# Kernel tuning notes

Measured on AMD Instinct MI355X. Metric: run time of the kernel, lower is better.

## Reference

```python
import jax, jax.numpy as jnp
import numpy as np

N_NODES, N_EDGES, H = 25000, 400000, 64
EPS = 1e-15


def _norm(x):
    return jnp.sqrt(jnp.sum(x * x, axis=-1, keepdims=True))


def _projx(x, c):
    norm = _norm(x)
    max_norm = (1.0 - 1e-5) / jnp.sqrt(c)
    scale = jnp.minimum(max_norm / jnp.maximum(norm, EPS), 1.0)
    return x * scale


def _expmap0(x, c):
    norm = _norm(x)
    sc = jnp.sqrt(c)
    return jnp.tanh(sc * norm) * x / (norm * sc + EPS)


def _logmap0(x, c):
    norm = _norm(x)
    sc = jnp.sqrt(c)
    return (1.0 / sc) * jnp.arctanh(jnp.minimum(sc * norm, 1.0 - 1e-5)) * x / (norm + EPS)


def _mobius_add(x, y, c):
    x2 = jnp.sum(x * x, axis=-1, keepdims=True)
    y2 = jnp.sum(y * y, axis=-1, keepdims=True)
    xy = jnp.sum(x * y, axis=-1, keepdims=True)
    num = (1.0 + 2.0 * c * xy + c * y2) * x + (1.0 - c * x2) * y
    denom = 1.0 + 2.0 * c * xy + c * c * x2 * y2
    return num / (denom + EPS)


def _mobius_linear(x, W, b, c):
    t = _logmap0(x, c)
    out = t @ W.T + b
    return _expmap0(out, c)


def setup_inputs() -> dict:
    key = jax.random.key(0)
    ks = jax.random.split(key, 12)
    h_V = jax.random.normal(ks[0], (N_NODES, H), dtype=jnp.float32) * 0.3
    h_E = jax.random.normal(ks[1], (N_EDGES, 3 * H), dtype=jnp.float32) * 0.3
    src = jax.random.randint(ks[2], (N_EDGES,), 0, N_NODES, dtype=jnp.int32)
    dst = jax.random.randint(ks[3], (N_EDGES,), 0, N_NODES, dtype=jnp.int32)
    log_c = jnp.zeros((), dtype=jnp.float32)  # c = 1.0

    def lin(k, out_d, in_d):
        bound = 1.0 / np.sqrt(in_d)
        kw, kb = jax.random.split(k)
        W = jax.random.uniform(kw, (out_d, in_d), jnp.float32, -bound, bound)
        b = jax.random.uniform(kb, (out_d,), jnp.float32, -bound, bound)
        return W, b

    W1_w, W1_b = lin(ks[4], H, 5 * H)
    W2_w, W2_b = lin(ks[5], H, H)
    W3_w, W3_b = lin(ks[6], H, H)
    return {"h_V": h_V, "h_E": h_E, "src": src, "dst": dst, "log_c": log_c,
            "W1_w": W1_w, "W1_b": W1_b, "W2_w": W2_w, "W2_b": W2_b,
            "W3_w": W3_w, "W3_b": W3_b}


def reference(h_V, h_E, src, dst, log_c, W1_w, W1_b, W2_w, W2_b, W3_w, W3_b):
    c = jnp.exp(log_c)
    n_nodes = h_V.shape[0]
    h_E = _projx(h_E, c)
    h_V = _projx(h_V, c)
    # edge gather -> fused mobius-linear chain  [E, 5H] -> [E, H]
    h_EV = jnp.concatenate([h_E, h_V[src], h_V[dst]], axis=-1)
    h_EV = _mobius_linear(h_EV, W1_w, W1_b, c)
    h_EV = _mobius_linear(_projx(jax.nn.relu(h_EV), c), W2_w, W2_b, c)
    h_msg = _mobius_linear(_projx(jax.nn.relu(h_EV), c), W3_w, W3_b, c)
    # hyperbolic aggregate: logmap0 -> scatter-mean over src -> expmap0
    tangent = _logmap0(h_msg, c)
    sums = jax.ops.segment_sum(tangent, src, num_segments=n_nodes)
    counts = jax.ops.segment_sum(jnp.ones((tangent.shape[0],), tangent.dtype), src,
                                 num_segments=n_nodes)
    agg_t = sums / jnp.maximum(counts, 1.0)[:, None]
    agg = _expmap0(agg_t, c)
    h_V = _mobius_add(h_V, agg, c)  # dropout disabled (eval)
    return _projx(h_V, c)
```

## Files before the change

### kernel.cpp

```cpp
#include <hip/hip_runtime.h>
#include <hip/hip_bf16.h>
#include <math.h>

#define EPSF 1e-15f

typedef __attribute__((ext_vector_type(8))) short bf16x8;
typedef __attribute__((ext_vector_type(4))) float f32x4;

__device__ __forceinline__ unsigned short f2bf(float x) {
    unsigned u = __float_as_uint(x);
    u += 0x7fffu + ((u >> 16) & 1u);
    return (unsigned short)(u >> 16);
}
__device__ __forceinline__ float bf2f(unsigned short b) {
    return __uint_as_float(((unsigned)b) << 16);
}
__device__ __forceinline__ unsigned pkbf(float lo, float hi) {
    __hip_bfloat162 h = __float22bfloat162_rn(make_float2(lo, hi));
    return *reinterpret_cast<unsigned*>(&h);
}
__device__ __forceinline__ float fast_tanh_pos(float x) {
    if (x < 0.25f) { float x2 = x * x; return x * (1.0f - x2 * (0.33333334f - 0.13333334f * x2)); }
    float e = __expf(2.0f * x);
    return 1.0f - 2.0f / (e + 1.0f);
}
__device__ __forceinline__ float fast_atanh01(float y) {
    if (y < 0.125f) { float y2 = y * y; return y * (1.0f + y2 * (0.33333334f + 0.2f * y2)); }
    return 0.5f * __logf((1.0f + y) / (1.0f - y));
}

__device__ __forceinline__ float wred(float v) {
#pragma unroll
    for (int off = 32; off; off >>= 1) v += __shfl_xor(v, off);
    return v;
}

__global__ void prep_wfrag(const float* __restrict__ W1, const float* __restrict__ W2,
                           const float* __restrict__ W3, unsigned short* __restrict__ Wf) {
    int idx = blockIdx.x * blockDim.x + threadIdx.x;
    if (idx >= 56 * 64) return;
    int fid = idx >> 6, lane = idx & 63;
    int i15 = lane & 15, grp = lane >> 4;
    const float* srcW; int ks, t, ld;
    if (fid < 40)      { srcW = W1; ks = fid >> 2;        t = fid & 3; ld = 320; }
    else if (fid < 48) { srcW = W2; ks = (fid - 40) >> 2; t = fid & 3; ld = 64; }
    else               { srcW = W3; ks = (fid - 48) >> 2; t = fid & 3; ld = 64; }
    int col = t * 16 + i15;
    int k0  = ks * 32 + grp * 8;
    unsigned short* dstp = Wf + ((size_t)fid * 64 + lane) * 8;
#pragma unroll
    for (int i = 0; i < 8; ++i) dstp[i] = f2bf(srcW[col * ld + k0 + i]);
}

__global__ void __launch_bounds__(256)
node_prep(const float* __restrict__ hV, const float* __restrict__ logc,
          unsigned short* __restrict__ hVp, float* __restrict__ pj, int n_nodes) {
    int wid  = (blockIdx.x * blockDim.x + threadIdx.x) >> 6;
    int lane = threadIdx.x & 63;
    if (wid >= n_nodes) return;
    float c    = __expf(logc[0]);
    float scq  = sqrtf(c);
    float maxn = (1.0f - 1e-5f) / scq;
    float x = hV[(size_t)wid * 64 + lane];
    float p = wred(x * x);
    float sS = fminf(maxn / fmaxf(sqrtf(p), EPSF), 1.0f);
    hVp[(size_t)wid * 64 + lane] = f2bf(x * sS);
    if (lane == 0) pj[wid] = sS * sS * p;
}

__global__ void hist_kernel(const int* __restrict__ src, int* __restrict__ cnt,
                            int* __restrict__ slot, int n_edges) {
    int e = blockIdx.x * blockDim.x + threadIdx.x;
    if (e < n_edges) slot[e] = atomicAdd(&cnt[src[e]], 1);
}

__global__ void __launch_bounds__(1024)
scan_rowptr(const int* __restrict__ cnt, int* __restrict__ rowptr, int n) {
    __shared__ int wpart[16];
    int C   = (n + 1023) >> 10;
    int tid = threadIdx.x;
    int beg = tid * C;
    int end = beg + C; if (end > n) end = n;
    int s = 0;
    if (beg < n) for (int k = beg; k < end; ++k) s += cnt[k];
    int lane = tid & 63, wv = tid >> 6;
    int v = s;
#pragma unroll
    for (int off = 1; off < 64; off <<= 1) {
        int t = __shfl_up(v, off);
        if (lane >= off) v += t;
    }
    if (lane == 63) wpart[wv] = v;
    __syncthreads();
    if (tid < 64) {
        int t = (tid < 16) ? wpart[tid] : 0;
#pragma unroll
        for (int off = 1; off < 16; off <<= 1) {
            int u = __shfl_up(t, off);
            if (lane >= off) t += u;
        }
        if (tid < 16) wpart[tid] = t;
    }
    __syncthreads();
    int base = (wv ? wpart[wv - 1] : 0) + (v - s);
    if (beg < n) {
        int run = base;
        for (int k = beg; k < end; ++k) { rowptr[k] = run; run += cnt[k]; }
    }
    if (tid == 1023) rowptr[n] = wpart[15];
}

__global__ void slotfix_kernel(const int* __restrict__ src, const int* __restrict__ rowptr,
                               int* __restrict__ slot, int n_edges) {
    int e = blockIdx.x * blockDim.x + threadIdx.x;
    if (e < n_edges) slot[e] += rowptr[src[e]];
}

__device__ __forceinline__ void stage_mlp(float (&v)[4][4], unsigned short* tb,
                                          const bf16x8* __restrict__ Wfrag, int fbase,
                                          const float* __restrict__ bvec,
                                          float scq, float maxn, int lane) {
    int i15 = lane & 15, grp = lane >> 4;
    float n2[4], rn2[4];
#pragma unroll
    for (int r = 0; r < 4; ++r) {
        float s = 0.f;
#pragma unroll
        for (int t = 0; t < 4; ++t) s = fmaf(v[t][r], v[t][r], s);
        n2[r] = s;
    }
#pragma unroll
    for (int r = 0; r < 4; ++r) {
        float s = 0.f;
        int row = grp * 4 + r;
#pragma unroll
        for (int t = 0; t < 4; ++t) {
            float u = fmaxf(v[t][r], 0.f);
            s = fmaf(u, u, s);
            int colc = t * 16 + i15;
            int unit = (colc >> 3) ^ (row & 7);
            tb[row * 64 + unit * 8 + (colc & 7)] = f2bf(u);
        }
        rn2[r] = s;
    }
#pragma unroll
    for (int m = 1; m <= 8; m <<= 1) {
#pragma unroll
        for (int r = 0; r < 4; ++r) {
            n2[r]  += __shfl_xor(n2[r], m);
            rn2[r] += __shfl_xor(rn2[r], m);
        }
    }
    float f2[4];
#pragma unroll
    for (int r = 0; r < 4; ++r) {
        float n  = sqrtf(n2[r]);
        float h  = fast_tanh_pos(scq * n) / (n * scq + EPSF);
        float rn = h * sqrtf(rn2[r]);
        float ps = fminf(maxn / fmaxf(rn, EPSF), 1.0f);
        float pn = rn * ps;
        float g  = fast_atanh01(fminf(scq * pn, 1.0f - 1e-5f)) / (scq * (pn + EPSF));
        f2[r] = h * ps * g;
    }
    asm volatile("s_waitcnt lgkmcnt(0)" ::: "memory");
    __builtin_amdgcn_sched_barrier(0);
    f32x4 acc[4] = {};
#pragma unroll
    for (int s2 = 0; s2 < 2; ++s2) {
        int unit = (s2 * 4 + grp) ^ (i15 & 7);
        bf16x8 a2 = *reinterpret_cast<const bf16x8*>(&tb[i15 * 64 + unit * 8]);
#pragma unroll
        for (int t = 0; t < 4; ++t)
            acc[t] = __builtin_amdgcn_mfma_f32_16x16x32_bf16(
                a2, Wfrag[(size_t)(fbase + s2 * 4 + t) * 64 + lane], acc[t], 0, 0, 0);
    }
#pragma unroll
    for (int t = 0; t < 4; ++t) {
        float bv = bvec[t * 16 + i15];
#pragma unroll
        for (int r = 0; r < 4; ++r) v[t][r] = fmaf(f2[r], acc[t][r], bv);
    }
}

__global__ void __launch_bounds__(256)
edge_mfma(const float* __restrict__ hE, const int* __restrict__ src,
          const int* __restrict__ dst, const float* __restrict__ logc,
          const unsigned short* __restrict__ Wf, const unsigned short* __restrict__ hVp,
          const float* __restrict__ pj,
          const float* __restrict__ b1, const float* __restrict__ b2,
          const float* __restrict__ b3, const int* __restrict__ slot,
          unsigned short* __restrict__ tg, int n_edges) {
    __shared__ __align__(16) float fbuf[4][16 * 68];
    int lane = threadIdx.x & 63;
    int w    = threadIdx.x >> 6;
    int tile = blockIdx.x * 4 + w;
    int e0 = tile * 16;
    if (e0 >= n_edges) return;

    float c    = __expf(logc[0]);
    float scq  = sqrtf(c);
    float maxn = (1.0f - 1e-5f) / scq;

    int i15 = lane & 15, grp = lane >> 4;
    int ev = e0 + i15; if (ev >= n_edges) ev = n_edges - 1;
    int s16 = src[ev], d16 = dst[ev];

    const bf16x8* Wfrag = reinterpret_cast<const bf16x8*>(Wf);

    const bf16x8* vsp = reinterpret_cast<const bf16x8*>(hVp + (size_t)s16 * 64);
    const bf16x8* vdp = reinterpret_cast<const bf16x8*>(hVp + (size_t)d16 * 64);
    bf16x8 aS0 = vsp[grp], aS1 = vsp[4 + grp];
    bf16x8 aD0 = vdp[grp], aD1 = vdp[4 + grp];
    float pjS = pj[s16], pjD = pj[d16];

    float pE = 0.f;
    bf16x8 aE[6];
    const float* eb = hE + (size_t)ev * 192;
#pragma unroll
    for (int ks = 0; ks < 6; ++ks) {
        const float4* p4 = reinterpret_cast<const float4*>(eb + ks * 32 + grp * 8);
        float4 a0 = p4[0], a1 = p4[1];
        pE += a0.x*a0.x + a0.y*a0.y + a0.z*a0.z + a0.w*a0.w
            + a1.x*a1.x + a1.y*a1.y + a1.z*a1.z + a1.w*a1.w;
        union { bf16x8 b; unsigned u[4]; } cv;
        cv.u[0] = pkbf(a0.x, a0.y);
        cv.u[1] = pkbf(a0.z, a0.w);
        cv.u[2] = pkbf(a1.x, a1.y);
        cv.u[3] = pkbf(a1.z, a1.w);
        aE[ks] = cv.b;
    }
    pE += __shfl_xor(pE, 16); pE += __shfl_xor(pE, 32);
    float sE = fminf(maxn / fmaxf(sqrtf(pE), EPSF), 1.0f);
    float nt = sqrtf(sE * sE * pE + pjS + pjD);
    float gq = fast_atanh01(fminf(scq * nt, 1.0f - 1e-5f)) / (scq * (nt + EPSF));

    f32x4 accE[4] = {}, accV[4] = {};
#pragma unroll
    for (int ks = 0; ks < 6; ++ks) {
#pragma unroll
        for (int t = 0; t < 4; ++t)
            accE[t] = __builtin_amdgcn_mfma_f32_16x16x32_bf16(
                aE[ks], Wfrag[(size_t)(ks * 4 + t) * 64 + lane], accE[t], 0, 0, 0);
    }
#pragma unroll
    for (int t = 0; t < 4; ++t)
        accV[t] = __builtin_amdgcn_mfma_f32_16x16x32_bf16(
            aS0, Wfrag[(size_t)(24 + t) * 64 + lane], accV[t], 0, 0, 0);
#pragma unroll
    for (int t = 0; t < 4; ++t)
        accV[t] = __builtin_amdgcn_mfma_f32_16x16x32_bf16(
            aS1, Wfrag[(size_t)(28 + t) * 64 + lane], accV[t], 0, 0, 0);
#pragma unroll
    for (int t = 0; t < 4; ++t)
        accV[t] = __builtin_amdgcn_mfma_f32_16x16x32_bf16(
            aD0, Wfrag[(size_t)(32 + t) * 64 + lane], accV[t], 0, 0, 0);
#pragma unroll
    for (int t = 0; t < 4; ++t)
        accV[t] = __builtin_amdgcn_mfma_f32_16x16x32_bf16(
            aD1, Wfrag[(size_t)(36 + t) * 64 + lane], accV[t], 0, 0, 0);

    float gr[4], ser[4];
#pragma unroll
    for (int r = 0; r < 4; ++r) {
        gr[r]  = __shfl(gq, grp * 4 + r);
        ser[r] = __shfl(sE, grp * 4 + r);
    }
    float v[4][4];
#pragma unroll
    for (int t = 0; t < 4; ++t) {
        float bv = b1[t * 16 + i15];
#pragma unroll
        for (int r = 0; r < 4; ++r)
            v[t][r] = fmaf(gr[r], fmaf(ser[r], accE[t][r], accV[t][r]), bv);
    }

    unsigned short* tb = reinterpret_cast<unsigned short*>(fbuf[w]);
    stage_mlp(v, tb, Wfrag, 40, b2, scq, maxn, lane);
    stage_mlp(v, tb, Wfrag, 48, b3, scq, maxn, lane);

    float n2f[4];
#pragma unroll
    for (int r = 0; r < 4; ++r) {
        float s = 0.f;
#pragma unroll
        for (int t = 0; t < 4; ++t) s = fmaf(v[t][r], v[t][r], s);
        n2f[r] = s;
    }
#pragma unroll
    for (int m = 1; m <= 8; m <<= 1) {
#pragma unroll
        for (int r = 0; r < 4; ++r) n2f[r] += __shfl_xor(n2f[r], m);
    }
    float fT[4];
#pragma unroll
    for (int r = 0; r < 4; ++r) {
        float n  = sqrtf(n2f[r]);
        float h  = fast_tanh_pos(scq * n) / (n * scq + EPSF);
        float hn = h * n;
        float g4 = fast_atanh01(fminf(scq * hn, 1.0f - 1e-5f)) / (scq * (hn + EPSF));
        fT[r] = g4 * h;
    }
    float* fb = fbuf[w];
    asm volatile("s_waitcnt lgkmcnt(0)" ::: "memory");
#pragma unroll
    for (int r = 0; r < 4; ++r) {
        int row = grp * 4 + r;
#pragma unroll
        for (int t = 0; t < 4; ++t) fb[row * 68 + t * 16 + i15] = fT[r] * v[t][r];
    }
    asm volatile("s_waitcnt lgkmcnt(0)" ::: "memory");
    __builtin_amdgcn_sched_barrier(0);
    int rowo = lane >> 2, cho = lane & 3;
    int eo = e0 + rowo;
    if (eo < n_edges) {
        int sl = slot[eo];
        float vals[16];
#pragma unroll
        for (int q = 0; q < 4; ++q) {
            f32x4 x = *reinterpret_cast<const f32x4*>(&fb[rowo * 68 + cho * 16 + q * 4]);
            vals[q*4+0] = x[0]; vals[q*4+1] = x[1]; vals[q*4+2] = x[2]; vals[q*4+3] = x[3];
        }
        unsigned pk[8];
#pragma unroll
        for (int i = 0; i < 8; ++i) pk[i] = pkbf(vals[2*i], vals[2*i+1]);
        uint4* op = reinterpret_cast<uint4*>(&tg[(size_t)sl * 64 + cho * 16]);
        op[0] = make_uint4(pk[0], pk[1], pk[2], pk[3]);
        op[1] = make_uint4(pk[4], pk[5], pk[6], pk[7]);
    }
}

__global__ void __launch_bounds__(256)
node_gather(const float* __restrict__ hV, const float* __restrict__ logc,
            const unsigned short* __restrict__ tg, const int* __restrict__ rowptr,
            float* __restrict__ out, int n_nodes) {
    int wid  = (blockIdx.x * blockDim.x + threadIdx.x) >> 6;
    int lane = threadIdx.x & 63;
    if (wid >= n_nodes) return;

    float c    = __expf(logc[0]);
    float scq  = sqrtf(c);
    float maxn = (1.0f - 1e-5f) / scq;

    int beg = rowptr[wid], end = rowptr[wid + 1];
    float ssum = 0.f;
    for (int i = beg; i < end; ++i)
        ssum += bf2f(tg[(size_t)i * 64 + lane]);
    float inv = 1.f / fmaxf((float)(end - beg), 1.f);
    float at  = ssum * inv;

    float an2 = wred(at * at);
    float an  = sqrtf(an2);
    float ae  = fast_tanh_pos(scq * an) / (an * scq + EPSF);

    float xv  = hV[(size_t)wid * 64 + lane];
    float hs2 = wred(xv * xv);
    float sX  = fminf(maxn / fmaxf(sqrtf(hs2), EPSF), 1.0f);

    float x = sX * xv, y = ae * at;
    float x2 = wred(x * x);
    float y2 = wred(y * y);
    float xy = wred(x * y);

    float ca = 1.f + 2.f * c * xy + c * y2;
    float cb = 1.f - c * x2;
    float id = 1.f / (1.f + 2.f * c * xy + c * c * x2 * y2 + EPSF);

    float r   = (ca * x + cb * y) * id;
    float rn2 = wred(r * r);
    float rs  = fminf(maxn / fmaxf(sqrtf(rn2), EPSF), 1.0f);

    out[(size_t)wid * 64 + lane] = rs * r;
}

extern "C" void kernel_launch(void* const* d_in, const int* in_sizes, int n_in,
                              void* d_out, int out_size, void* d_ws, size_t ws_size,
                              hipStream_t stream) {
    const float* hV   = (const float*)d_in[0];
    const float* hE   = (const float*)d_in[1];
    const int*   src  = (const int*)d_in[2];
    const int*   dst  = (const int*)d_in[3];
    const float* logc = (const float*)d_in[4];
    const float* W1   = (const float*)d_in[5];
    const float* b1   = (const float*)d_in[6];
    const float* W2   = (const float*)d_in[7];
    const float* b2   = (const float*)d_in[8];
    const float* W3   = (const float*)d_in[9];
    const float* b3   = (const float*)d_in[10];

    int n_nodes = in_sizes[0] / 64;
    int n_edges = in_sizes[2];
    float* out = (float*)d_out;

    char* wsb = (char*)d_ws;
    unsigned short* Wf = (unsigned short*)wsb;
    size_t off = 56 * 512 * sizeof(unsigned short);
    int* cnt    = (int*)(wsb + off);   off += (size_t)n_nodes * 4;
    int* rowptr = (int*)(wsb + off);   off += (size_t)(n_nodes + 1) * 4;
    int* slot   = (int*)(wsb + off);   off += (size_t)n_edges * 4;
    float* pj   = (float*)(wsb + off); off += (size_t)n_nodes * 4;
    off = (off + 15) & ~(size_t)15;
    unsigned short* hVp = (unsigned short*)(wsb + off);
    off += (size_t)n_nodes * 64 * 2;
    off = (off + 15) & ~(size_t)15;
    unsigned short* tg = (unsigned short*)(wsb + off);

    hipMemsetAsync(cnt, 0, (size_t)n_nodes * sizeof(int), stream);

    prep_wfrag<<<(56 * 64 + 255) / 256, 256, 0, stream>>>(W1, W2, W3, Wf);
    node_prep<<<(n_nodes + 3) / 4, 256, 0, stream>>>(hV, logc, hVp, pj, n_nodes);
    hist_kernel<<<(n_edges + 255) / 256, 256, 0, stream>>>(src, cnt, slot, n_edges);
    scan_rowptr<<<1, 1024, 0, stream>>>(cnt, rowptr, n_nodes);
    slotfix_kernel<<<(n_edges + 255) / 256, 256, 0, stream>>>(src, rowptr, slot, n_edges);

    int tiles = (n_edges + 15) / 16;
    edge_mfma<<<(tiles + 3) / 4, 256, 0, stream>>>(
        hE, src, dst, logc, Wf, hVp, pj, b1, b2, b3, slot, tg, n_edges);

    node_gather<<<(n_nodes + 3) / 4, 256, 0, stream>>>(
        hV, logc, tg, rowptr, out, n_nodes);
}
```

Measured before the change: 267.2 us.

## Transpose MFMA orientation to keep edge rows per lane, drop LDS staging

Swaps the MFMA operand order so the weight fragment is the A operand and the activations are B. Each lane then holds the features of a single edge, so per-row norms need only two cross-group shuffles, and the next stage's input can be packed in registers instead of going through swizzled LDS. The W2/W3 fragment layout is permuted to match. The LDS transpose before the output write is removed, and each lane writes 8-byte chunks directly. node_gather now processes four edges at a time using 4-element vector loads. The risks are narrower, less coalesced output stores and the correctness of the permuted-K fragment layout.

Result: faster. 237.4 us (-11.1%).

```diff
diff --git a/kernel.cpp b/kernel.cpp
--- a/kernel.cpp
+++ b/kernel.cpp
@@ -41,15 +41,24 @@
     if (idx >= 56 * 64) return;
     int fid = idx >> 6, lane = idx & 63;
     int i15 = lane & 15, grp = lane >> 4;
-    const float* srcW; int ks, t, ld;
-    if (fid < 40)      { srcW = W1; ks = fid >> 2;        t = fid & 3; ld = 320; }
-    else if (fid < 48) { srcW = W2; ks = (fid - 40) >> 2; t = fid & 3; ld = 64; }
-    else               { srcW = W3; ks = (fid - 48) >> 2; t = fid & 3; ld = 64; }
-    int col = t * 16 + i15;
-    int k0  = ks * 32 + grp * 8;
     unsigned short* dstp = Wf + ((size_t)fid * 64 + lane) * 8;
-#pragma unroll
-    for (int i = 0; i < 8; ++i) dstp[i] = f2bf(srcW[col * ld + k0 + i]);
+    if (fid < 40) {
+        int ks = fid >> 2, t = fid & 3;
+        int n = t * 16 + i15;
+        int k0 = ks * 32 + grp * 8;
+#pragma unroll
+        for (int i = 0; i < 8; ++i) dstp[i] = f2bf(W1[n * 320 + k0 + i]);
+    } else {
+        const float* srcW = (fid < 48) ? W2 : W3;
+        int b = (fid < 48) ? fid - 40 : fid - 48;
+        int s2 = b >> 2, t = b & 3;
+        int n = t * 16 + i15;
+#pragma unroll
+        for (int i = 0; i < 8; ++i) {
+            int kp = 16 * (2 * s2 + (i >> 2)) + 4 * grp + (i & 3);
+            dstp[i] = f2bf(srcW[n * 64 + kp]);
+        }
+    }
 }
 
 __global__ void __launch_bounds__(256)
@@ -116,69 +125,55 @@
     if (e < n_edges) slot[e] += rowptr[src[e]];
 }
 
-__device__ __forceinline__ void stage_mlp(float (&v)[4][4], unsigned short* tb,
-                                          const bf16x8* __restrict__ Wfrag, int fbase,
-                                          const float* __restrict__ bvec,
-                                          float scq, float maxn, int lane) {
-    int i15 = lane & 15, grp = lane >> 4;
-    float n2[4], rn2[4];
-#pragma unroll
-    for (int r = 0; r < 4; ++r) {
-        float s = 0.f;
-#pragma unroll
-        for (int t = 0; t < 4; ++t) s = fmaf(v[t][r], v[t][r], s);
-        n2[r] = s;
-    }
-#pragma unroll
-    for (int r = 0; r < 4; ++r) {
-        float s = 0.f;
-        int row = grp * 4 + r;
-#pragma unroll
-        for (int t = 0; t < 4; ++t) {
-            float u = fmaxf(v[t][r], 0.f);
-            s = fmaf(u, u, s);
-            int colc = t * 16 + i15;
-            int unit = (colc >> 3) ^ (row & 7);
-            tb[row * 64 + unit * 8 + (colc & 7)] = f2bf(u);
+__device__ __forceinline__ void stage_mlp_t(float (&v)[4][4],
+                                            const bf16x8* __restrict__ Wfrag, int fbase,
+                                            const float* __restrict__ bvec,
+                                            float scq, float maxn, int grp) {
+    float n2 = 0.f, rn2 = 0.f;
+    float u[4][4];
+#pragma unroll
+    for (int t = 0; t < 4; ++t)
+#pragma unroll
+        for (int r = 0; r < 4; ++r) {
+            float x = v[t][r];
+            n2 = fmaf(x, x, n2);
+            float y = fmaxf(x, 0.f);
+            u[t][r] = y;
+            rn2 = fmaf(y, y, rn2);
         }
-        rn2[r] = s;
-    }
-#pragma unroll
-    for (int m = 1; m <= 8; m <<= 1) {
-#pragma unroll
-        for (int r = 0; r < 4; ++r) {
-            n2[r]  += __shfl_xor(n2[r], m);
-            rn2[r] += __shfl_xor(rn2[r], m);
-        }
-    }
-    float f2[4];
-#pragma unroll
-    for (int r = 0; r < 4; ++r) {
-        float n  = sqrtf(n2[r]);
-        float h  = fast_tanh_pos(scq * n) / (n * scq + EPSF);
-        float rn = h * sqrtf(rn2[r]);
-        float ps = fminf(maxn / fmaxf(rn, EPSF), 1.0f);
-        float pn = rn * ps;
-        float g  = fast_atanh01(fminf(scq * pn, 1.0f - 1e-5f)) / (scq * (pn + EPSF));
-        f2[r] = h * ps * g;
-    }
-    asm volatile("s_waitcnt lgkmcnt(0)" ::: "memory");
-    __builtin_amdgcn_sched_barrier(0);
+    n2  += __shfl_xor(n2, 16);  n2  += __shfl_xor(n2, 32);
+    rn2 += __shfl_xor(rn2, 16); rn2 += __shfl_xor(rn2, 32);
+    float n  = sqrtf(n2);
+    float h  = fast_tanh_pos(scq * n) / (n * scq + EPSF);
+    float rn = h * sqrtf(rn2);
+    float ps = fminf(maxn / fmaxf(rn, EPSF), 1.0f);
+    float pn = rn * ps;
+    float gg = fast_atanh01(fminf(scq * pn, 1.0f - 1e-5f)) / (scq * (pn + EPSF));
+    float f2 = h * ps * gg;
+
+    union { bf16x8 b; unsigned w[4]; } B0, B1;
+    B0.w[0] = pkbf(u[0][0], u[0][1]); B0.w[1] = pkbf(u[0][2], u[0][3]);
+    B0.w[2] = pkbf(u[1][0], u[1][1]); B0.w[3] = pkbf(u[1][2], u[1][3]);
+    B1.w[0] = pkbf(u[2][0], u[2][1]); B1.w[1] = pkbf(u[2][2], u[2][3]);
+    B1.w[2] = pkbf(u[3][0], u[3][1]); B1.w[3] = pkbf(u[3][2], u[3][3]);
+
     f32x4 acc[4] = {};
 #pragma unroll
-    for (int s2 = 0; s2 < 2; ++s2) {
-        int unit = (s2 * 4 + grp) ^ (i15 & 7);
-        bf16x8 a2 = *reinterpret_cast<const bf16x8*>(&tb[i15 * 64 + unit * 8]);
-#pragma unroll
-        for (int t = 0; t < 4; ++t)
-            acc[t] = __builtin_amdgcn_mfma_f32_16x16x32_bf16(
-                a2, Wfrag[(size_t)(fbase + s2 * 4 + t) * 64 + lane], acc[t], 0, 0, 0);
-    }
+    for (int t = 0; t < 4; ++t)
+        acc[t] = __builtin_amdgcn_mfma_f32_16x16x32_bf16(
+            Wfrag[(size_t)(fbase + t) * 64 + (grp * 16 + (threadIdx.x & 15))], B0.b, acc[t], 0, 0, 0);
+#pragma unroll
+    for (int t = 0; t < 4; ++t)
+        acc[t] = __builtin_amdgcn_mfma_f32_16x16x32_bf16(
+            Wfrag[(size_t)(fbase + 4 + t) * 64 + (grp * 16 + (threadIdx.x & 15))], B1.b, acc[t], 0, 0, 0);
+
 #pragma unroll
     for (int t = 0; t < 4; ++t) {
-        float bv = bvec[t * 16 + i15];
-#pragma unroll
-        for (int r = 0; r < 4; ++r) v[t][r] = fmaf(f2[r], acc[t][r], bv);
+        const float4 bv = *reinterpret_cast<const float4*>(&bvec[t * 16 + 4 * grp]);
+        v[t][0] = fmaf(f2, acc[t][0], bv.x);
+        v[t][1] = fmaf(f2, acc[t][1], bv.y);
+        v[t][2] = fmaf(f2, acc[t][2], bv.z);
+        v[t][3] = fmaf(f2, acc[t][3], bv.w);
     }
 }
 
@@ -190,7 +185,6 @@
           const float* __restrict__ b1, const float* __restrict__ b2,
           const float* __restrict__ b3, const int* __restrict__ slot,
           unsigned short* __restrict__ tg, int n_edges) {
-    __shared__ __align__(16) float fbuf[4][16 * 68];
     int lane = threadIdx.x & 63;
     int w    = threadIdx.x >> 6;
     int tile = blockIdx.x * 4 + w;
@@ -240,92 +234,60 @@
 #pragma unroll
         for (int t = 0; t < 4; ++t)
             accE[t] = __builtin_amdgcn_mfma_f32_16x16x32_bf16(
-                aE[ks], Wfrag[(size_t)(ks * 4 + t) * 64 + lane], accE[t], 0, 0, 0);
+                Wfrag[(size_t)(ks * 4 + t) * 64 + lane], aE[ks], accE[t], 0, 0, 0);
     }
 #pragma unroll
     for (int t = 0; t < 4; ++t)
         accV[t] = __builtin_amdgcn_mfma_f32_16x16x32_bf16(
-            aS0, Wfrag[(size_t)(24 + t) * 64 + lane], accV[t], 0, 0, 0);
+            Wfrag[(size_t)(24 + t) * 64 + lane], aS0, accV[t], 0, 0, 0);
 #pragma unroll
     for (int t = 0; t < 4; ++t)
         accV[t] = __builtin_amdgcn_mfma_f32_16x16x32_bf16(
-            aS1, Wfrag[(size_t)(28 + t) * 64 + lane], accV[t], 0, 0, 0);
+            Wfrag[(size_t)(28 + t) * 64 + lane], aS1, accV[t], 0, 0, 0);
 #pragma unroll
     for (int t = 0; t < 4; ++t)
         accV[t] = __builtin_amdgcn_mfma_f32_16x16x32_bf16(
-            aD0, Wfrag[(size_t)(32 + t) * 64 + lane], accV[t], 0, 0, 0);
+            Wfrag[(size_t)(32 + t) * 64 + lane], aD0, accV[t], 0, 0, 0);
 #pragma unroll
     for (int t = 0; t < 4; ++t)
         accV[t] = __builtin_amdgcn_mfma_f32_16x16x32_bf16(
-            aD1, Wfrag[(size_t)(36 + t) * 64 + lane], accV[t], 0, 0, 0);
-
-    float gr[4], ser[4];
-#pragma unroll
-    for (int r = 0; r < 4; ++r) {
-        gr[r]  = __shfl(gq, grp * 4 + r);
-        ser[r] = __shfl(sE, grp * 4 + r);
-    }
+            Wfrag[(size_t)(36 + t) * 64 + lane], aD1, accV[t], 0, 0, 0);
+
     float v[4][4];
 #pragma unroll
     for (int t = 0; t < 4; ++t) {
-        float bv = b1[t * 16 + i15];
-#pragma unroll
-        for (int r = 0; r < 4; ++r)
-            v[t][r] = fmaf(gr[r], fmaf(ser[r], accE[t][r], accV[t][r]), bv);
-    }
-
-    unsigned short* tb = reinterpret_cast<unsigned short*>(fbuf[w]);
-    stage_mlp(v, tb, Wfrag, 40, b2, scq, maxn, lane);
-    stage_mlp(v, tb, Wfrag, 48, b3, scq, maxn, lane);
-
-    float n2f[4];
-#pragma unroll
-    for (int r = 0; r < 4; ++r) {
-        float s = 0.f;
-#pragma unroll
-        for (int t = 0; t < 4; ++t) s = fmaf(v[t][r], v[t][r], s);
-        n2f[r] = s;
-    }
-#pragma unroll
-    for (int m = 1; m <= 8; m <<= 1) {
-#pragma unroll
-        for (int r = 0; r < 4; ++r) n2f[r] += __shfl_xor(n2f[r], m);
-    }
-    float fT[4];
-#pragma unroll
-    for (int r = 0; r < 4; ++r) {
-        float n  = sqrtf(n2f[r]);
-        float h  = fast_tanh_pos(scq * n) / (n * scq + EPSF);
-        float hn = h * n;
-        float g4 = fast_atanh01(fminf(scq * hn, 1.0f - 1e-5f)) / (scq * (hn + EPSF));
-        fT[r] = g4 * h;
-    }
-    float* fb = fbuf[w];
-    asm volatile("s_waitcnt lgkmcnt(0)" ::: "memory");
-#pragma unroll
-    for (int r = 0; r < 4; ++r) {
-        int row = grp * 4 + r;
-#pragma unroll
-        for (int t = 0; t < 4; ++t) fb[row * 68 + t * 16 + i15] = fT[r] * v[t][r];
-    }
-    asm volatile("s_waitcnt lgkmcnt(0)" ::: "memory");
-    __builtin_amdgcn_sched_barrier(0);
-    int rowo = lane >> 2, cho = lane & 3;
-    int eo = e0 + rowo;
-    if (eo < n_edges) {
-        int sl = slot[eo];
-        float vals[16];
-#pragma unroll
-        for (int q = 0; q < 4; ++q) {
-            f32x4 x = *reinterpret_cast<const f32x4*>(&fb[rowo * 68 + cho * 16 + q * 4]);
-            vals[q*4+0] = x[0]; vals[q*4+1] = x[1]; vals[q*4+2] = x[2]; vals[q*4+3] = x[3];
+        const float4 bv = *reinterpret_cast<const float4*>(&b1[t * 16 + 4 * grp]);
+        v[t][0] = fmaf(gq, fmaf(sE, accE[t][0], accV[t][0]), bv.x);
+        v[t][1] = fmaf(gq, fmaf(sE, accE[t][1], accV[t][1]), bv.y);
+        v[t][2] = fmaf(gq, fmaf(sE, accE[t][2], accV[t][2]), bv.z);
+        v[t][3] = fmaf(gq, fmaf(sE, accE[t][3], accV[t][3]), bv.w);
+    }
+
+    stage_mlp_t(v, Wfrag, 40, b2, scq, maxn, grp);
+    stage_mlp_t(v, Wfrag, 48, b3, scq, maxn, grp);
+
+    float n2 = 0.f;
+#pragma unroll
+    for (int t = 0; t < 4; ++t)
+#pragma unroll
+        for (int r = 0; r < 4; ++r) n2 = fmaf(v[t][r], v[t][r], n2);
+    n2 += __shfl_xor(n2, 16); n2 += __shfl_xor(n2, 32);
+    float n  = sqrtf(n2);
+    float h  = fast_tanh_pos(scq * n) / (n * scq + EPSF);
+    float hn = h * n;
+    float g4 = fast_atanh01(fminf(scq * hn, 1.0f - 1e-5f)) / (scq * (hn + EPSF));
+    float fT = g4 * h;
+
+    if (e0 + i15 < n_edges) {
+        int sl = slot[ev];
+        unsigned short* orow = tg + (size_t)sl * 64;
+#pragma unroll
+        for (int t = 0; t < 4; ++t) {
+            uint2 o;
+            o.x = pkbf(fT * v[t][0], fT * v[t][1]);
+            o.y = pkbf(fT * v[t][2], fT * v[t][3]);
+            *reinterpret_cast<uint2*>(&orow[t * 16 + 4 * grp]) = o;
         }
-        unsigned pk[8];
-#pragma unroll
-        for (int i = 0; i < 8; ++i) pk[i] = pkbf(vals[2*i], vals[2*i+1]);
-        uint4* op = reinterpret_cast<uint4*>(&tg[(size_t)sl * 64 + cho * 16]);
-        op[0] = make_uint4(pk[0], pk[1], pk[2], pk[3]);
-        op[1] = make_uint4(pk[4], pk[5], pk[6], pk[7]);
     }
 }
 
@@ -342,9 +304,24 @@
     float maxn = (1.0f - 1e-5f) / scq;
 
     int beg = rowptr[wid], end = rowptr[wid + 1];
-    float ssum = 0.f;
-    for (int i = beg; i < end; ++i)
-        ssum += bf2f(tg[(size_t)i * 64 + lane]);
+    int g = lane >> 4, i15 = lane & 15;
+    float s0 = 0.f, s1 = 0.f, s2 = 0.f, s3 = 0.f;
+    for (int i = beg + g; i < end; i += 4) {
+        uint2 p = *reinterpret_cast<const uint2*>(&tg[(size_t)i * 64 + i15 * 4]);
+        s0 += bf2f((unsigned short)(p.x & 0xffff));
+        s1 += bf2f((unsigned short)(p.x >> 16));
+        s2 += bf2f((unsigned short)(p.y & 0xffff));
+        s3 += bf2f((unsigned short)(p.y >> 16));
+    }
+    s0 += __shfl_xor(s0, 16); s0 += __shfl_xor(s0, 32);
+    s1 += __shfl_xor(s1, 16); s1 += __shfl_xor(s1, 32);
+    s2 += __shfl_xor(s2, 16); s2 += __shfl_xor(s2, 32);
+    s3 += __shfl_xor(s3, 16); s3 += __shfl_xor(s3, 32);
+    int srcl = lane >> 2;
+    float a0 = __shfl(s0, srcl), a1 = __shfl(s1, srcl);
+    float a2 = __shfl(s2, srcl), a3 = __shfl(s3, srcl);
+    float ssum = (lane & 2) ? ((lane & 1) ? a3 : a2) : ((lane & 1) ? a1 : a0);
+
     float inv = 1.f / fmaxf((float)(end - beg), 1.f);
     float at  = ssum * inv;
 
```
